# Kernel optimization log

Measured on AMD Instinct MI355X. Metric: run time of the kernel, lower is better.

## Reference

```python
import jax, jax.numpy as jnp
import numpy as np

N_NODES = 100000
N_EDGES = 800000
HIDDEN = 128


def setup_inputs() -> dict:
    key = jax.random.key(0)
    ks = jax.random.split(key, 9)
    h_n = jax.random.normal(ks[0], (N_NODES, HIDDEN), dtype=jnp.float32)
    edge_src = jax.random.randint(ks[1], (N_EDGES,), 0, N_NODES, dtype=jnp.int32)
    edge_dst = jax.random.randint(ks[2], (N_EDGES,), 0, N_NODES, dtype=jnp.int32)
    s = 0.05
    W_w = jax.random.normal(ks[3], (HIDDEN, HIDDEN), dtype=jnp.float32) * s
    W_b = jax.random.normal(ks[4], (HIDDEN,), dtype=jnp.float32) * s
    Ws_w = jax.random.normal(ks[5], (HIDDEN, HIDDEN), dtype=jnp.float32) * s
    Ws_b = jax.random.normal(ks[6], (HIDDEN,), dtype=jnp.float32) * s
    Wt_w = jax.random.normal(ks[7], (HIDDEN, HIDDEN), dtype=jnp.float32) * s
    Wt_b = jax.random.normal(ks[8], (HIDDEN,), dtype=jnp.float32) * s
    return {"h_n": h_n, "edge_src": edge_src, "edge_dst": edge_dst,
            "W_w": W_w, "W_b": W_b, "Ws_w": Ws_w, "Ws_b": Ws_b,
            "Wt_w": Wt_w, "Wt_b": Wt_b}


def reference(h_n, edge_src, edge_dst, W_w, W_b, Ws_w, Ws_b, Wt_w, Wt_b):
    # Dense linears (nn.Linear: x @ W.T + b)
    Wh = h_n @ W_w.T + W_b        # [N,H] used for A @ W(h)
    Wsh = h_n @ Ws_w.T + Ws_b     # [N,H] self term
    Wth = h_n @ Wt_w.T + Wt_b     # [N,H] used for A.T @ W_trans(h)
    # A[src,dst] = 1:  (A @ X)[i]   = sum over edges (i,j) of X[j]
    #              (A.T @ X)[j] = sum over edges (i,j) of X[i]
    agg_fwd = jax.ops.segment_sum(Wh[edge_dst], edge_src, num_segments=N_NODES)
    agg_bwd = jax.ops.segment_sum(Wth[edge_src], edge_dst, num_segments=N_NODES)
    return jax.nn.relu(agg_fwd + Wsh + agg_bwd)
```

## Files before the change

kernel.cpp:

```cpp
#include <hip/hip_runtime.h>
#include <hip/hip_bf16.h>

#define NN 100000
#define NE 800000
#define HIDDEN 128
#define NED (2 * NE)
#define BKN 128
#define NBF 782
#define NBUCK (2 * NBF)
#define CHUNK 8192
#define PBLK ((NED + CHUNK - 1) / CHUNK)
#define NTILES 3125

typedef __attribute__((ext_vector_type(8))) short bf16x8;
typedef __attribute__((ext_vector_type(4))) short bf16x4;
typedef __attribute__((ext_vector_type(4))) float f32x4;

__device__ __forceinline__ short f2bf(float f) {
  union { float f; unsigned u; } x; x.f = f;
  unsigned r = x.u + 0x7fffu + ((x.u >> 16) & 1u);
  return (short)(r >> 16);
}
__device__ __forceinline__ float bf2f(short s) {
  union { unsigned u; float f; } x;
  x.u = ((unsigned)(unsigned short)s) << 16;
  return x.f;
}

__global__ __launch_bounds__(256) void convert_weights(
    const float* __restrict__ m0, const float* __restrict__ m1,
    const float* __restrict__ m2, short* __restrict__ out) {
  int i = blockIdx.x * 256 + threadIdx.x;
  int m = i >> 14, j = i & 16383;
  const float* s = (m == 0) ? m0 : (m == 1) ? m1 : m2;
  out[i] = f2bf(s[j]);
}

__global__ __launch_bounds__(256) void convert_h(
    const float* __restrict__ h, short* __restrict__ h_bf) {
  int i = blockIdx.x * 256 + threadIdx.x;
  f32x4 v = *(const f32x4*)(h + (size_t)i * 4);
  bf16x4 o;
#pragma unroll
  for (int j = 0; j < 4; j++) o[j] = f2bf(v[j]);
  *(bf16x4*)(h_bf + (size_t)i * 4) = o;
}

__global__ __launch_bounds__(256) void part_count(
    const int* __restrict__ esrc, const int* __restrict__ edst,
    int* __restrict__ ghist) {
  __shared__ int lh[NBUCK];
  int tid = threadIdx.x;
  for (int i = tid; i < NBUCK; i += 256) lh[i] = 0;
  __syncthreads();
  int base = blockIdx.x * CHUNK;
  int nit = min(CHUNK, NED - base);
  for (int k = tid; k < nit; k += 256) {
    int ed = base + k;
    int b;
    if (ed < NE) b = esrc[ed] >> 7;
    else b = NBF + (edst[ed - NE] >> 7);
    atomicAdd(&lh[b], 1);
  }
  __syncthreads();
  for (int i = tid; i < NBUCK; i += 256) {
    int c = lh[i];
    if (c) atomicAdd(ghist + i, c);
  }
}

__global__ __launch_bounds__(1024) void bucket_scan(
    const int* __restrict__ ghist, int* __restrict__ bstart,
    int* __restrict__ gcur) {
  __shared__ int lds[1024];
  __shared__ int carry;
  int tid = threadIdx.x;
  if (tid == 0) carry = 0;
  __syncthreads();
  for (int t = 0; t < 2; t++) {
    int i = t * 1024 + tid;
    int v = (i < NBUCK) ? ghist[i] : 0;
    lds[tid] = v;
    __syncthreads();
    for (int off = 1; off < 1024; off <<= 1) {
      int x = lds[tid];
      int add = (tid >= off) ? lds[tid - off] : 0;
      __syncthreads();
      lds[tid] = x + add;
      __syncthreads();
    }
    int excl = lds[tid] - v + carry;
    if (i < NBUCK) { bstart[i] = excl; gcur[i] = excl; }
    int tot = lds[1023];
    __syncthreads();
    if (tid == 0) carry += tot;
    __syncthreads();
  }
  if (tid == 0) bstart[NBUCK] = carry;
}

__global__ __launch_bounds__(256) void part_scatter(
    const int* __restrict__ esrc, const int* __restrict__ edst,
    int* __restrict__ gcur, unsigned* __restrict__ ELP) {
  __shared__ int lh[NBUCK];
  __shared__ int loff[NBUCK];
  __shared__ int lcur[NBUCK];
  __shared__ int gbase[NBUCK];
  __shared__ int psum[256];
  __shared__ unsigned buf[CHUNK];
  int tid = threadIdx.x;
  for (int i = tid; i < NBUCK; i += 256) lh[i] = 0;
  __syncthreads();
  int base = blockIdx.x * CHUNK;
  int nit = min(CHUNK, NED - base);
  for (int k = tid; k < nit; k += 256) {
    int ed = base + k;
    int b;
    if (ed < NE) b = esrc[ed] >> 7;
    else b = NBF + (edst[ed - NE] >> 7);
    atomicAdd(&lh[b], 1);
  }
  __syncthreads();
  int s = 0;
  int lo0 = tid * 7, hi0 = min(NBUCK, tid * 7 + 7);
  for (int j = lo0; j < hi0; j++) s += lh[j];
  psum[tid] = s;
  __syncthreads();
  for (int off = 1; off < 256; off <<= 1) {
    int x = psum[tid];
    int add = (tid >= off) ? psum[tid - off] : 0;
    __syncthreads();
    psum[tid] = x + add;
    __syncthreads();
  }
  int run = psum[tid] - s;
  for (int j = lo0; j < hi0; j++) { loff[j] = run; lcur[j] = run; run += lh[j]; }
  __syncthreads();
  for (int b = tid; b < NBUCK; b += 256) {
    int c = lh[b];
    if (c) gbase[b] = atomicAdd(gcur + b, c);
  }
  __syncthreads();
  for (int k = tid; k < nit; k += 256) {
    int ed = base + k;
    int b, tl, nbr;
    if (ed < NE) { int tg = esrc[ed]; nbr = edst[ed]; b = tg >> 7; tl = tg & 127; }
    else { int e = ed - NE; int tg = edst[e]; nbr = esrc[e]; b = NBF + (tg >> 7); tl = tg & 127; }
    int slot = atomicAdd(&lcur[b], 1);
    buf[slot] = ((unsigned)tl << 17) | (unsigned)nbr;
  }
  __syncthreads();
  for (int i = tid; i < nit; i += 256) {
    int lo = 0, hi = NBUCK - 1;
    while (lo < hi) {
      int mid = (lo + hi + 1) >> 1;
      if (loff[mid] <= i) lo = mid; else hi = mid - 1;
    }
    ELP[gbase[lo] + (i - loff[lo])] = buf[i];
  }
}

__global__ __launch_bounds__(256) void bucket_gather(
    const short* __restrict__ h_bf, const unsigned* __restrict__ ELP,
    const int* __restrict__ bstart,
    short* __restrict__ aggF, short* __restrict__ aggB,
    int* __restrict__ degFB) {
  __shared__ int sorted[2048];
  __shared__ int cnt[BKN];
  __shared__ int pfx[BKN];
  __shared__ int cur[BKN];
  int tid = threadIdx.x;
  int blk = blockIdx.x;
  int s = bstart[blk], e = bstart[blk + 1], n = e - s;
  if (tid < BKN) cnt[tid] = 0;
  __syncthreads();
  for (int k = tid; k < n; k += 256) atomicAdd(&cnt[ELP[s + k] >> 17], 1);
  __syncthreads();
  int v = (tid < BKN) ? cnt[tid] : 0;
  if (tid < BKN) pfx[tid] = v;
  __syncthreads();
  for (int off = 1; off < BKN; off <<= 1) {
    int add = (tid < BKN && tid >= off) ? pfx[tid - off] : 0;
    __syncthreads();
    if (tid < BKN) pfx[tid] += add;
    __syncthreads();
  }
  if (tid < BKN) cur[tid] = pfx[tid] - cnt[tid];
  __syncthreads();
  for (int k = tid; k < n; k += 256) {
    unsigned pv = ELP[s + k];
    int slot = atomicAdd(&cur[pv >> 17], 1);
    sorted[slot] = (int)(pv & 0x1FFFFu);
  }
  __syncthreads();
  int dir = blk >= NBF;
  int node0 = (dir ? blk - NBF : blk) * BKN;
  short* agg = dir ? aggB : aggF;
  int hw = tid >> 5, q = tid & 31;
  for (int t = 0; t < 16; t++) {
    int nd = hw * 16 + t;
    int b = pfx[nd];
    int a = b - cnt[nd];
    float a0 = 0.f, a1 = 0.f, a2 = 0.f, a3 = 0.f;
    if (a < b) {
      int nbr = sorted[a];
      for (int j = a + 1; j < b; j++) {
        int nxt = sorted[j];
        bf16x4 vv = *(const bf16x4*)(h_bf + (size_t)nbr * HIDDEN + q * 4);
        a0 += bf2f(vv[0]); a1 += bf2f(vv[1]); a2 += bf2f(vv[2]); a3 += bf2f(vv[3]);
        nbr = nxt;
      }
      bf16x4 vv = *(const bf16x4*)(h_bf + (size_t)nbr * HIDDEN + q * 4);
      a0 += bf2f(vv[0]); a1 += bf2f(vv[1]); a2 += bf2f(vv[2]); a3 += bf2f(vv[3]);
    }
    int node = node0 + nd;
    if (node < NN) {
      bf16x4 o;
      o[0] = f2bf(a0); o[1] = f2bf(a1); o[2] = f2bf(a2); o[3] = f2bf(a3);
      *(bf16x4*)(agg + (size_t)node * HIDDEN + q * 4) = o;
    }
  }
  if (tid < BKN) {
    int node = node0 + tid;
    if (node < NN) degFB[dir * NN + node] = cnt[tid];
  }
}

__global__ __launch_bounds__(512, 4) void gemm_fused(
    const short* __restrict__ h_bf, const short* __restrict__ aggF,
    const short* __restrict__ aggB, const short* __restrict__ Wbf,
    const float* __restrict__ Wb, const float* __restrict__ Wsb,
    const float* __restrict__ Wtb, const int* __restrict__ degFB,
    float* __restrict__ out) {
  __shared__ short At[3 * 32 * 136];
  int tid = threadIdx.x;
  int lane = tid & 63;
  int m16 = lane & 15;
  int kq  = lane >> 4;
  int col0 = (tid >> 6) * 16;

  bf16x8 wf[3][4];
#pragma unroll
  for (int i = 0; i < 3; i++)
#pragma unroll
    for (int t = 0; t < 4; t++)
      wf[i][t] = *(const bf16x8*)(Wbf + i * 16384 + (col0 + m16) * 128 + t * 32 + kq * 8);

  f32x4 bW = *(const f32x4*)(Wb  + col0 + kq * 4);
  f32x4 bS = *(const f32x4*)(Wsb + col0 + kq * 4);
  f32x4 bT = *(const f32x4*)(Wtb + col0 + kq * 4);

  int srow = tid >> 4, skc = tid & 15;
  const short* mats[3] = { h_bf, aggF, aggB };
  const short* gbs[3];
  short* lps[3];
#pragma unroll
  for (int k = 0; k < 3; k++) {
    gbs[k] = mats[k] + srow * 128 + skc * 8;
    lps[k] = At + k * 4352 + srow * 136 + skc * 8;
  }

  int tile = blockIdx.x;
  bf16x8 ld[3];
#pragma unroll
  for (int k = 0; k < 3; k++)
    ld[k] = *(const bf16x8*)(gbs[k] + (size_t)tile * 4096);

  while (tile < NTILES) {
    int row0 = tile * 32;
    __syncthreads();
#pragma unroll
    for (int k = 0; k < 3; k++) *(bf16x8*)lps[k] = ld[k];
    __syncthreads();
    int ntile = tile + gridDim.x;
    if (ntile < NTILES) {
#pragma unroll
      for (int k = 0; k < 3; k++)
        ld[k] = *(const bf16x8*)(gbs[k] + (size_t)ntile * 4096);
    }
#pragma unroll
    for (int g = 0; g < 2; g++) {
      f32x4 acc = {0.f, 0.f, 0.f, 0.f};
      const short* lb = At + (g * 16 + m16) * 136 + kq * 8;
#pragma unroll
      for (int i = 0; i < 3; i++)
#pragma unroll
        for (int t = 0; t < 4; t++) {
          bf16x8 af = *(const bf16x8*)(lb + i * 4352 + t * 32);
          acc = __builtin_amdgcn_mfma_f32_16x16x32_bf16(wf[i][t], af, acc, 0, 0, 0);
        }
      int r = row0 + g * 16 + m16;
      float dF = (float)degFB[r];
      float dB = (float)degFB[NN + r];
      f32x4 v;
#pragma unroll
      for (int j = 0; j < 4; j++)
        v[j] = fmaxf(acc[j] + bS[j] + dF * bW[j] + dB * bT[j], 0.f);
      *(f32x4*)(out + (size_t)r * HIDDEN + col0 + kq * 4) = v;
    }
    tile = ntile;
  }
}

extern "C" void kernel_launch(void* const* d_in, const int* in_sizes, int n_in,
                              void* d_out, int out_size, void* d_ws, size_t ws_size,
                              hipStream_t stream) {
  const float* h    = (const float*)d_in[0];
  const int*   esrc = (const int*)d_in[1];
  const int*   edst = (const int*)d_in[2];
  const float* Ww   = (const float*)d_in[3];
  const float* Wb   = (const float*)d_in[4];
  const float* Wsw  = (const float*)d_in[5];
  const float* Wsb  = (const float*)d_in[6];
  const float* Wtw  = (const float*)d_in[7];
  const float* Wtb  = (const float*)d_in[8];
  float* out = (float*)d_out;

  char* ws = (char*)d_ws;
  int*      ghist  = (int*)(ws + 0);
  int*      bstart = (int*)(ws + 6272);
  int*      gcur   = (int*)(ws + 12544);
  unsigned* ELP    = (unsigned*)(ws + 18816);
  short*    Wbf    = (short*)(ws + 6418816);
  short*    h_bf   = (short*)(ws + 6517120);
  short*    aggF   = (short*)(ws + 32117120);
  short*    aggB   = (short*)(ws + 57717120);
  int*      degFB  = (int*)(ws + 83317120);

  hipMemsetAsync(ghist, 0, NBUCK * sizeof(int), stream);

  convert_weights<<<192, 256, 0, stream>>>(Wsw, Ww, Wtw, Wbf);
  convert_h<<<12500, 256, 0, stream>>>(h, h_bf);
  part_count<<<PBLK, 256, 0, stream>>>(esrc, edst, ghist);
  bucket_scan<<<1, 1024, 0, stream>>>(ghist, bstart, gcur);
  part_scatter<<<PBLK, 256, 0, stream>>>(esrc, edst, gcur, ELP);
  bucket_gather<<<NBUCK, 256, 0, stream>>>(h_bf, ELP, bstart, aggF, aggB, degFB);
  gemm_fused<<<1024, 512, 0, stream>>>(
      h_bf, aggF, aggB, Wbf, Wb, Wsb, Wtb, degFB, out);
}
```

Baseline: 281.7 us.

## Halve bucket size, store bucket ids in scatter, unroll gather with 8-wide loads

Shrinks node buckets from 128 to 64 nodes, doubling the number of gather blocks, and adjusts the scan and prefix partitioning to match. The scatter kernel now records each slot's bucket id in shared memory, which replaces the per-element binary search when writing to global memory. The gather loop uses 16 lanes per node with 8-element bf16 loads and keeps four neighbor rows in flight, handling the remainder with masked FMAs. The aim is more parallelism and more memory-level parallelism in the gather. The cost is more shared memory in part_scatter and more buckets to scan.

```diff
diff --git a/kernel.cpp b/kernel.cpp
--- a/kernel.cpp
+++ b/kernel.cpp
@@ -5,9 +5,10 @@
 #define NE 800000
 #define HIDDEN 128
 #define NED (2 * NE)
-#define BKN 128
-#define NBF 782
+#define BKN 64
+#define NBF 1563
 #define NBUCK (2 * NBF)
+#define PS 13
 #define CHUNK 8192
 #define PBLK ((NED + CHUNK - 1) / CHUNK)
 #define NTILES 3125
@@ -58,8 +59,8 @@
   for (int k = tid; k < nit; k += 256) {
     int ed = base + k;
     int b;
-    if (ed < NE) b = esrc[ed] >> 7;
-    else b = NBF + (edst[ed - NE] >> 7);
+    if (ed < NE) b = esrc[ed] >> 6;
+    else b = NBF + (edst[ed - NE] >> 6);
     atomicAdd(&lh[b], 1);
   }
   __syncthreads();
@@ -77,7 +78,7 @@
   int tid = threadIdx.x;
   if (tid == 0) carry = 0;
   __syncthreads();
-  for (int t = 0; t < 2; t++) {
+  for (int t = 0; t < 4; t++) {
     int i = t * 1024 + tid;
     int v = (i < NBUCK) ? ghist[i] : 0;
     lds[tid] = v;
@@ -108,6 +109,7 @@
   __shared__ int gbase[NBUCK];
   __shared__ int psum[256];
   __shared__ unsigned buf[CHUNK];
+  __shared__ unsigned short bidA[CHUNK];
   int tid = threadIdx.x;
   for (int i = tid; i < NBUCK; i += 256) lh[i] = 0;
   __syncthreads();
@@ -116,13 +118,13 @@
   for (int k = tid; k < nit; k += 256) {
     int ed = base + k;
     int b;
-    if (ed < NE) b = esrc[ed] >> 7;
-    else b = NBF + (edst[ed - NE] >> 7);
+    if (ed < NE) b = esrc[ed] >> 6;
+    else b = NBF + (edst[ed - NE] >> 6);
     atomicAdd(&lh[b], 1);
   }
   __syncthreads();
   int s = 0;
-  int lo0 = tid * 7, hi0 = min(NBUCK, tid * 7 + 7);
+  int lo0 = tid * PS, hi0 = min(NBUCK, tid * PS + PS);
   for (int j = lo0; j < hi0; j++) s += lh[j];
   psum[tid] = s;
   __syncthreads();
@@ -144,28 +146,31 @@
   for (int k = tid; k < nit; k += 256) {
     int ed = base + k;
     int b, tl, nbr;
-    if (ed < NE) { int tg = esrc[ed]; nbr = edst[ed]; b = tg >> 7; tl = tg & 127; }
-    else { int e = ed - NE; int tg = edst[e]; nbr = esrc[e]; b = NBF + (tg >> 7); tl = tg & 127; }
+    if (ed < NE) { int tg = esrc[ed]; nbr = edst[ed]; b = tg >> 6; tl = tg & 63; }
+    else { int e = ed - NE; int tg = edst[e]; nbr = esrc[e]; b = NBF + (tg >> 6); tl = tg & 63; }
     int slot = atomicAdd(&lcur[b], 1);
     buf[slot] = ((unsigned)tl << 17) | (unsigned)nbr;
+    bidA[slot] = (unsigned short)b;
   }
   __syncthreads();
   for (int i = tid; i < nit; i += 256) {
-    int lo = 0, hi = NBUCK - 1;
-    while (lo < hi) {
-      int mid = (lo + hi + 1) >> 1;
-      if (loff[mid] <= i) lo = mid; else hi = mid - 1;
-    }
-    ELP[gbase[lo] + (i - loff[lo])] = buf[i];
-  }
-}
-
-__global__ __launch_bounds__(256) void bucket_gather(
+    int b = bidA[i];
+    ELP[gbase[b] + (i - loff[b])] = buf[i];
+  }
+}
+
+#define ACC8(V) { a0f+=bf2f((V)[0]); a1f+=bf2f((V)[1]); a2f+=bf2f((V)[2]); a3f+=bf2f((V)[3]); \
+                  a4f+=bf2f((V)[4]); a5f+=bf2f((V)[5]); a6f+=bf2f((V)[6]); a7f+=bf2f((V)[7]); }
+#define MACC8(M,V) { a0f=fmaf(M,bf2f((V)[0]),a0f); a1f=fmaf(M,bf2f((V)[1]),a1f); \
+                     a2f=fmaf(M,bf2f((V)[2]),a2f); a3f=fmaf(M,bf2f((V)[3]),a3f); \
+                     a4f=fmaf(M,bf2f((V)[4]),a4f); a5f=fmaf(M,bf2f((V)[5]),a5f); \
+                     a6f=fmaf(M,bf2f((V)[6]),a6f); a7f=fmaf(M,bf2f((V)[7]),a7f); }
+__global__ __launch_bounds__(256, 6) void bucket_gather(
     const short* __restrict__ h_bf, const unsigned* __restrict__ ELP,
     const int* __restrict__ bstart,
     short* __restrict__ aggF, short* __restrict__ aggB,
     int* __restrict__ degFB) {
-  __shared__ int sorted[2048];
+  __shared__ int sorted[1024];
   __shared__ int cnt[BKN];
   __shared__ int pfx[BKN];
   __shared__ int cur[BKN];
@@ -196,28 +201,54 @@
   int dir = blk >= NBF;
   int node0 = (dir ? blk - NBF : blk) * BKN;
   short* agg = dir ? aggB : aggF;
-  int hw = tid >> 5, q = tid & 31;
-  for (int t = 0; t < 16; t++) {
-    int nd = hw * 16 + t;
-    int b = pfx[nd];
-    int a = b - cnt[nd];
-    float a0 = 0.f, a1 = 0.f, a2 = 0.f, a3 = 0.f;
-    if (a < b) {
-      int nbr = sorted[a];
-      for (int j = a + 1; j < b; j++) {
-        int nxt = sorted[j];
-        bf16x4 vv = *(const bf16x4*)(h_bf + (size_t)nbr * HIDDEN + q * 4);
-        a0 += bf2f(vv[0]); a1 += bf2f(vv[1]); a2 += bf2f(vv[2]); a3 += bf2f(vv[3]);
-        nbr = nxt;
+  int qw = tid >> 4, q = tid & 15;
+  const short* hb = h_bf + (size_t)q * 8;
+#pragma unroll
+  for (int t = 0; t < 4; t++) {
+    int nd = qw * 4 + t;
+    int b0 = pfx[nd];
+    int deg = cnt[nd];
+    int a0 = b0 - deg;
+    float a0f = 0.f, a1f = 0.f, a2f = 0.f, a3f = 0.f;
+    float a4f = 0.f, a5f = 0.f, a6f = 0.f, a7f = 0.f;
+    if (deg > 0) {
+      int lastp = b0 - 1;
+      int i0 = sorted[a0];
+      int i1 = sorted[min(a0 + 1, lastp)];
+      int i2 = sorted[min(a0 + 2, lastp)];
+      int i3 = sorted[min(a0 + 3, lastp)];
+      bf16x8 v0 = *(const bf16x8*)(hb + (size_t)i0 * HIDDEN);
+      bf16x8 v1 = *(const bf16x8*)(hb + (size_t)i1 * HIDDEN);
+      bf16x8 v2 = *(const bf16x8*)(hb + (size_t)i2 * HIDDEN);
+      bf16x8 v3 = *(const bf16x8*)(hb + (size_t)i3 * HIDDEN);
+      int j = a0;
+      int ni0 = sorted[min(j + 4, lastp)];
+      int ni1 = sorted[min(j + 5, lastp)];
+      int ni2 = sorted[min(j + 6, lastp)];
+      int ni3 = sorted[min(j + 7, lastp)];
+      while (j + 4 <= b0) {
+        ACC8(v0); v0 = *(const bf16x8*)(hb + (size_t)ni0 * HIDDEN);
+        ACC8(v1); v1 = *(const bf16x8*)(hb + (size_t)ni1 * HIDDEN);
+        ACC8(v2); v2 = *(const bf16x8*)(hb + (size_t)ni2 * HIDDEN);
+        ACC8(v3); v3 = *(const bf16x8*)(hb + (size_t)ni3 * HIDDEN);
+        j += 4;
+        ni0 = sorted[min(j + 4, lastp)];
+        ni1 = sorted[min(j + 5, lastp)];
+        ni2 = sorted[min(j + 6, lastp)];
+        ni3 = sorted[min(j + 7, lastp)];
       }
-      bf16x4 vv = *(const bf16x4*)(h_bf + (size_t)nbr * HIDDEN + q * 4);
-      a0 += bf2f(vv[0]); a1 += bf2f(vv[1]); a2 += bf2f(vv[2]); a3 += bf2f(vv[3]);
+      int r = b0 - j;
+      float m1 = (r > 0) ? 1.f : 0.f;
+      float m2 = (r > 1) ? 1.f : 0.f;
+      float m3 = (r > 2) ? 1.f : 0.f;
+      MACC8(m1, v0); MACC8(m2, v1); MACC8(m3, v2);
     }
     int node = node0 + nd;
     if (node < NN) {
-      bf16x4 o;
-      o[0] = f2bf(a0); o[1] = f2bf(a1); o[2] = f2bf(a2); o[3] = f2bf(a3);
-      *(bf16x4*)(agg + (size_t)node * HIDDEN + q * 4) = o;
+      bf16x8 o;
+      o[0] = f2bf(a0f); o[1] = f2bf(a1f); o[2] = f2bf(a2f); o[3] = f2bf(a3f);
+      o[4] = f2bf(a4f); o[5] = f2bf(a5f); o[6] = f2bf(a6f); o[7] = f2bf(a7f);
+      *(bf16x8*)(agg + (size_t)node * HIDDEN + q * 8) = o;
     }
   }
   if (tid < BKN) {
@@ -318,14 +349,14 @@
 
   char* ws = (char*)d_ws;
   int*      ghist  = (int*)(ws + 0);
-  int*      bstart = (int*)(ws + 6272);
-  int*      gcur   = (int*)(ws + 12544);
-  unsigned* ELP    = (unsigned*)(ws + 18816);
-  short*    Wbf    = (short*)(ws + 6418816);
-  short*    h_bf   = (short*)(ws + 6517120);
-  short*    aggF   = (short*)(ws + 32117120);
-  short*    aggB   = (short*)(ws + 57717120);
-  int*      degFB  = (int*)(ws + 83317120);
+  int*      bstart = (int*)(ws + 12544);
+  int*      gcur   = (int*)(ws + 25088);
+  unsigned* ELP    = (unsigned*)(ws + 37632);
+  short*    Wbf    = (short*)(ws + 6437632);
+  short*    h_bf   = (short*)(ws + 6535936);
+  short*    aggF   = (short*)(ws + 32135936);
+  short*    aggB   = (short*)(ws + 57735936);
+  int*      degFB  = (int*)(ws + 83335936);
 
   hipMemsetAsync(ghist, 0, NBUCK * sizeof(int), stream);
 
```

After: 264.4 us. 1.07x faster.
